# Kernel optimization log

Hardware: AMD Instinct MI355X
Metric: run time of the kernel (lower is better)

## Reference

```python
import jax, jax.numpy as jnp
import numpy as np


def setup_inputs() -> dict:
    N, E, D = 50000, 800000, 64
    key = jax.random.key(0)
    ks = jax.random.split(key, 8)
    s = 1.0 / np.sqrt(2 * D)
    inp = {
        "node_emb": jax.random.normal(ks[0], (N, D), dtype=jnp.float32),
        "edge_index": jax.random.randint(ks[1], (2, E), 0, N, dtype=jnp.int64),
        "W1": jax.random.normal(ks[2], (2 * D, D), dtype=jnp.float32) * s,
        "b1": jnp.zeros((D,), dtype=jnp.float32),
        "W2": jax.random.normal(ks[3], (D, D), dtype=jnp.float32) * (1.0 / np.sqrt(D)),
        "b2": jnp.zeros((D,), dtype=jnp.float32),
        "Wg": jax.random.normal(ks[4], (D, D), dtype=jnp.float32) * (1.0 / np.sqrt(D)),
        "bg": jnp.zeros((D,), dtype=jnp.float32),
    }
    return inp


def reference(node_emb, edge_index, W1, b1, W2, b2, Wg, bg):
    # Gather pairwise embeddings along edges
    src, dst = edge_index[0], edge_index[1]
    pair_emb = jnp.concatenate([node_emb[src], node_emb[dst]], axis=-1)  # [E, 2D]
    # Interaction MLP (dropout in eval mode -> identity)
    h = jax.nn.relu(pair_emb @ W1 + b1)
    interaction = h @ W2 + b2  # [E, D]
    # Sigmoid gate
    gate = jax.nn.sigmoid(interaction @ Wg + bg)
    gated = interaction * gate  # [E, D]
    # Scatter-mean back to source nodes
    N = node_emb.shape[0]
    summed = jax.ops.segment_sum(gated, src, num_segments=N)  # [N, D]
    counts = jax.ops.segment_sum(jnp.ones((src.shape[0],), dtype=gated.dtype), src, num_segments=N)
    pooled = summed / jnp.maximum(counts, 1.0)[:, None]
    return pooled
```

## Files before the change

### kernel.cpp

```cpp
#include <hip/hip_runtime.h>


typedef unsigned short ushort_t;
typedef __attribute__((ext_vector_type(8))) short     bf16x8;
typedef __attribute__((ext_vector_type(8))) unsigned short u16x8;
typedef __attribute__((ext_vector_type(4))) float     f32x4;

constexpr int D        = 64;
constexpr int TILE     = 64;
constexpr int BLOCK    = 256;
constexpr int PAIR_STR = 136;
constexpr int H_STR    = 72;
constexpr int G_STR    = 68;
constexpr int NFRAG    = 32;

static __device__ __forceinline__ ushort_t f2bf(float f) {
    union { float f; unsigned int u; } v; v.f = f;
    const unsigned int r = v.u + 0x7FFFu + ((v.u >> 16) & 1u);
    return (ushort_t)(r >> 16);
}


__global__ void prep_kernel(const float* __restrict__ W1, const float* __restrict__ W2,
                            const float* __restrict__ Wg,
                            const float* __restrict__ b2, const float* __restrict__ bg,
                            const float* __restrict__ emb, const int* __restrict__ ei,
                            ushort_t* __restrict__ wpack, float* __restrict__ bgp,
                            ushort_t* __restrict__ emb_bf, int* __restrict__ cnt,
                            int total_emb, int cvt_blocks, int E) {
    const int bid = blockIdx.x;
    if (bid < 64) {
        const int t = bid * 256 + threadIdx.x;
        const int f = t >> 9;
        const int l = (t >> 3) & 63;
        const int j = t & 7;
        const int k = ((f < 16) ? (f & 3) : ((f - 16) & 1)) * 32 + (l >> 4) * 8 + j;
        const int n = ((f < 16) ? (f >> 2) : (((f & 7)) >> 1)) * 16 + (l & 15);
        float v;
        if (f < 16)      v = W1[k * 64 + n];
        else if (f < 24) v = W2[k * 64 + n];
        else {
            float s = 0.f;
            const float* wr = W2 + k * 64;
#pragma unroll 8
            for (int m = 0; m < 64; ++m) s += wr[m] * Wg[m * 64 + n];
            v = s;
        }
        wpack[t] = f2bf(v);
    } else if (bid < 64 + cvt_blocks) {
        const int idx  = (bid - 64) * 256 + threadIdx.x;
        const int base = idx * 8;
        if (base < total_emb) {
            const float4 a = *(const float4*)(emb + base);
            const float4 b = *(const float4*)(emb + base + 4);
            u16x8 p;
            p[0]=f2bf(a.x); p[1]=f2bf(a.y); p[2]=f2bf(a.z); p[3]=f2bf(a.w);
            p[4]=f2bf(b.x); p[5]=f2bf(b.y); p[6]=f2bf(b.z); p[7]=f2bf(b.w);
            *(u16x8*)(emb_bf + base) = p;
        }
    } else if (bid == 64 + cvt_blocks) {
        const int n = threadIdx.x;
        if (n < 64) {
            float s = bg[n];
#pragma unroll 8
            for (int m = 0; m < 64; ++m) s += b2[m] * Wg[m * 64 + n];
            bgp[n] = s;
        }
    } else {
        const int e = ((bid - 65 - cvt_blocks) * 256 + threadIdx.x) * 4;
        if (e + 3 < E) {
            const int4 v = *(const int4*)(ei + e);
            atomicAdd(&cnt[v.x], 1); atomicAdd(&cnt[v.y], 1);
            atomicAdd(&cnt[v.z], 1); atomicAdd(&cnt[v.w], 1);
        } else {
            for (int k = e; k < E; ++k) atomicAdd(&cnt[ei[k]], 1);
        }
    }
}


__global__ void scan_block(const int* __restrict__ cnt, int* __restrict__ off,
                           int* __restrict__ bsum, int N) {
    __shared__ int s[256];
    const int t = threadIdx.x, i = blockIdx.x * 256 + t;
    const int x = (i < N) ? cnt[i] : 0;
    s[t] = x; __syncthreads();
    for (int d = 1; d < 256; d <<= 1) {
        const int v = (t >= d) ? s[t - d] : 0;
        __syncthreads();
        s[t] += v;
        __syncthreads();
    }
    if (i < N) off[i] = s[t] - x;
    if (t == 255) bsum[blockIdx.x] = s[255];
}

__global__ void scan_sums(int* __restrict__ bsum, int nb) {
    __shared__ int s[256];
    const int t = threadIdx.x;
    const int x = (t < nb) ? bsum[t] : 0;
    s[t] = x; __syncthreads();
    for (int d = 1; d < 256; d <<= 1) {
        const int v = (t >= d) ? s[t - d] : 0;
        __syncthreads();
        s[t] += v;
        __syncthreads();
    }
    if (t < nb) bsum[t] = s[t] - x;
}

__global__ void add_sums(int* __restrict__ off, const int* __restrict__ bsum, int N) {
    const int i = blockIdx.x * 256 + threadIdx.x;
    if (i < N) off[i] += bsum[blockIdx.x];
}

__global__ void scatter_idx(const int* __restrict__ ei, int* __restrict__ off,
                            int* __restrict__ sorted, int E) {
    const int e = (blockIdx.x * blockDim.x + threadIdx.x) * 4;
    if (e + 3 < E) {
        const int4 v = *(const int4*)(ei + e);
        sorted[atomicAdd(&off[v.x], 1)] = e;
        sorted[atomicAdd(&off[v.y], 1)] = e + 1;
        sorted[atomicAdd(&off[v.z], 1)] = e + 2;
        sorted[atomicAdd(&off[v.w], 1)] = e + 3;
    } else {
        for (int k = e; k < E; ++k) sorted[atomicAdd(&off[ei[k]], 1)] = k;
    }
}


__global__ __launch_bounds__(BLOCK, 5)
void edge_mlp_mfma(const ushort_t* __restrict__ emb_bf,
                   const int*   __restrict__ edge_index,
                   const int*   __restrict__ sorted,
                   const ushort_t* __restrict__ wpack,
                   const float* __restrict__ b1, const float* __restrict__ b2,
                   const float* __restrict__ bgp,
                   float* __restrict__ summed,
                   int E)
{
    __shared__ union {
        ushort_t pairA[TILE][PAIR_STR];
        float    gated[TILE][G_STR];
    } u;
    __shared__ ushort_t hA[TILE][H_STR];
    __shared__ int      srcIds[TILE];

    const int tid = threadIdx.x;

    {
        const int e = tid >> 2, q = tid & 3;
        const int ide = blockIdx.x * TILE + e;
        if (ide < E) {
            const int eg = sorted[ide];
            const int s  = edge_index[eg];
            const int dn = edge_index[E + eg];
            if (q == 0) srcIds[e] = s;
            const ushort_t* sr = emb_bf + (size_t)s  * D + q * 16;
            const ushort_t* dr = emb_bf + (size_t)dn * D + q * 16;
            *(u16x8*)&u.pairA[e][q * 16]          = *(const u16x8*)sr;
            *(u16x8*)&u.pairA[e][q * 16 + 8]      = *(const u16x8*)(sr + 8);
            *(u16x8*)&u.pairA[e][64 + q * 16]     = *(const u16x8*)dr;
            *(u16x8*)&u.pairA[e][64 + q * 16 + 8] = *(const u16x8*)(dr + 8);
        } else {
            if (q == 0) srcIds[e] = -1;
            const u16x8 z = {0,0,0,0,0,0,0,0};
            *(u16x8*)&u.pairA[e][q * 16]          = z;
            *(u16x8*)&u.pairA[e][q * 16 + 8]      = z;
            *(u16x8*)&u.pairA[e][64 + q * 16]     = z;
            *(u16x8*)&u.pairA[e][64 + q * 16 + 8] = z;
        }
    }

    const int w    = tid >> 6;
    const int ln   = tid & 63;
    const int quad = ln >> 4;
    const int cn   = ln & 15;
    const int mrow = 16 * w + cn;
    const int orow = 16 * w + quad * 4;

    bf16x8 a1f[4];
#pragma unroll
    for (int kc = 0; kc < 4; ++kc)
        a1f[kc] = *(const bf16x8*)&u.pairA[mrow][kc * 32 + quad * 8];

    f32x4 acc1[4];
#pragma unroll
    for (int nt = 0; nt < 4; ++nt) {
        const float b = b1[nt * 16 + cn];
        acc1[nt] = (f32x4){b, b, b, b};
    }
#pragma unroll
    for (int nt = 0; nt < 4; ++nt)
#pragma unroll
        for (int kc = 0; kc < 4; ++kc) {
            const bf16x8 bf = *(const bf16x8*)(wpack + ((nt * 4 + kc) * 64 + ln) * 8);
            acc1[nt] = __builtin_amdgcn_mfma_f32_16x16x32_bf16(a1f[kc], bf, acc1[nt], 0, 0, 0);
        }
#pragma unroll
    for (int nt = 0; nt < 4; ++nt)
#pragma unroll
        for (int r = 0; r < 4; ++r)
            hA[orow + r][nt * 16 + cn] = f2bf(fmaxf(acc1[nt][r], 0.f));

    bf16x8 a2f[2];
#pragma unroll
    for (int kc = 0; kc < 2; ++kc)
        a2f[kc] = *(const bf16x8*)&hA[mrow][kc * 32 + quad * 8];

    f32x4 acc2[4], accg[4];
#pragma unroll
    for (int nt = 0; nt < 4; ++nt) {
        const float b  = b2 [nt * 16 + cn];
        const float bG = bgp[nt * 16 + cn];
        acc2[nt] = (f32x4){b, b, b, b};
        accg[nt] = (f32x4){bG, bG, bG, bG};
    }
#pragma unroll
    for (int nt = 0; nt < 4; ++nt)
#pragma unroll
        for (int kc = 0; kc < 2; ++kc) {
            const bf16x8 bf2 = *(const bf16x8*)(wpack + ((16 + nt * 2 + kc) * 64 + ln) * 8);
            const bf16x8 bfg = *(const bf16x8*)(wpack + ((24 + nt * 2 + kc) * 64 + ln) * 8);
            acc2[nt] = __builtin_amdgcn_mfma_f32_16x16x32_bf16(a2f[kc], bf2, acc2[nt], 0, 0, 0);
            accg[nt] = __builtin_amdgcn_mfma_f32_16x16x32_bf16(a2f[kc], bfg, accg[nt], 0, 0, 0);
        }

#pragma unroll
    for (int nt = 0; nt < 4; ++nt)
#pragma unroll
        for (int r = 0; r < 4; ++r) {
            const float g = 1.0f / (1.0f + __expf(-accg[nt][r]));
            u.gated[orow + r][nt * 16 + cn] = acc2[nt][r] * g;
        }

    {
        const int rbase = 16 * w;
        float run = 0.f;
        int   prev = srcIds[rbase];
#pragma unroll
        for (int i = 0; i < 16; ++i) {
            const int s = srcIds[rbase + i];
            const float v = u.gated[rbase + i][ln];
            if (s != prev) {
                if (prev >= 0) unsafeAtomicAdd(&summed[(size_t)prev * D + ln], run);
                run = 0.f;
                prev = s;
            }
            run += v;
        }
        if (prev >= 0) unsafeAtomicAdd(&summed[(size_t)prev * D + ln], run);
    }
}

__global__ void finalize_mean(float* __restrict__ out,
                              const int* __restrict__ cnt,
                              int total)
{
    const int b = (blockIdx.x * blockDim.x + threadIdx.x) * 4;
    if (b < total) {
        float4 v = *(float4*)&out[b];
        const float c = fmaxf((float)cnt[b >> 6], 1.0f);
        v.x /= c; v.y /= c; v.z /= c; v.w /= c;
        *(float4*)&out[b] = v;
    }
}

extern "C" void kernel_launch(void* const* d_in, const int* in_sizes, int n_in,
                              void* d_out, int out_size, void* d_ws, size_t ws_size,
                              hipStream_t stream) {
    const float* node_emb   = (const float*)d_in[0];
    const int*   edge_index = (const int*)d_in[1];
    const float* W1 = (const float*)d_in[2];
    const float* b1 = (const float*)d_in[3];
    const float* W2 = (const float*)d_in[4];
    const float* b2 = (const float*)d_in[5];
    const float* Wg = (const float*)d_in[6];
    const float* bg = (const float*)d_in[7];

    const int N = in_sizes[0] / D;
    const int E = in_sizes[1] / 2;
    const int total_emb = N * D;

    int* cnt    = (int*)d_ws;
    int* off    = cnt + N;
    int* bsum   = off + N;
    int* sorted = bsum + 256;
    float* bgp  = (float*)(sorted + E);
    ushort_t* wpack  = (ushort_t*)(bgp + 64);
    ushort_t* emb_bf = wpack + NFRAG * 512;

    float* summed = (float*)d_out;

    hipMemsetAsync(cnt, 0, sizeof(int) * (size_t)N, stream);
    hipMemsetAsync(summed, 0, sizeof(float) * (size_t)total_emb, stream);

    const int cvt_blocks = (total_emb / 8 + 255) / 256;
    const int e4blocks   = ((E + 3) / 4 + 255) / 256;
    prep_kernel<<<64 + cvt_blocks + 1 + e4blocks, 256, 0, stream>>>(
        W1, W2, Wg, b2, bg, node_emb, edge_index,
        wpack, bgp, emb_bf, cnt, total_emb, cvt_blocks, E);

    const int nblocks = (N + 255) / 256;
    scan_block <<<nblocks, 256, 0, stream>>>(cnt, off, bsum, N);
    scan_sums  <<<1,       256, 0, stream>>>(bsum, nblocks);
    add_sums   <<<nblocks, 256, 0, stream>>>(off, bsum, N);
    scatter_idx<<<e4blocks, 256, 0, stream>>>(edge_index, off, sorted, E);

    const int ntiles = (E + TILE - 1) / TILE;
    edge_mlp_mfma<<<ntiles, BLOCK, 0, stream>>>(emb_bf, edge_index, sorted, wpack,
                                                b1, b2, bgp, summed, E);

    finalize_mean<<<(total_emb / 4 + 255) / 256, 256, 0, stream>>>(summed, cnt, total_emb);
}
```

Measured before the change: 263.0 us.

## Fuse scan passes into scatter, fold mean into edge kernel, shrink LDS per warp

Removes the scan_sums and add_sums kernels: each scatter_idx block now recomputes the block-sum prefix in shared memory and adds it to the per-block local offset. The finalize_mean pass is dropped by scaling each partial sum by the reciprocal source count before the atomic add. The edge MLP's shared memory becomes per-warp slabs reused for pair, hidden and gated data, and launch bounds rise from 5 to 8 blocks to allow more occupancy. This trades several launches and one full pass over the output for redundant per-block scans and possible register pressure.

```diff
diff --git a/kernel.cpp b/kernel.cpp
--- a/kernel.cpp
+++ b/kernel.cpp
@@ -9,10 +9,11 @@
 constexpr int D        = 64;
 constexpr int TILE     = 64;
 constexpr int BLOCK    = 256;
+constexpr int NFRAG    = 32;
+constexpr int SLAB_B   = 4352;
 constexpr int PAIR_STR = 136;
 constexpr int H_STR    = 72;
 constexpr int G_STR    = 68;
-constexpr int NFRAG    = 32;
 
 static __device__ __forceinline__ ushort_t f2bf(float f) {
     union { float f; unsigned int u; } v; v.f = f;
@@ -95,80 +96,75 @@
     if (t == 255) bsum[blockIdx.x] = s[255];
 }
 
-__global__ void scan_sums(int* __restrict__ bsum, int nb) {
-    __shared__ int s[256];
+__global__ void scatter_idx(const int* __restrict__ ei, int* __restrict__ off,
+                            const int* __restrict__ bsum, int* __restrict__ sorted,
+                            int E, int nb) {
+    __shared__ int pref[256];
     const int t = threadIdx.x;
     const int x = (t < nb) ? bsum[t] : 0;
-    s[t] = x; __syncthreads();
+    pref[t] = x; __syncthreads();
     for (int d = 1; d < 256; d <<= 1) {
-        const int v = (t >= d) ? s[t - d] : 0;
-        __syncthreads();
-        s[t] += v;
-        __syncthreads();
-    }
-    if (t < nb) bsum[t] = s[t] - x;
-}
-
-__global__ void add_sums(int* __restrict__ off, const int* __restrict__ bsum, int N) {
-    const int i = blockIdx.x * 256 + threadIdx.x;
-    if (i < N) off[i] += bsum[blockIdx.x];
-}
-
-__global__ void scatter_idx(const int* __restrict__ ei, int* __restrict__ off,
-                            int* __restrict__ sorted, int E) {
-    const int e = (blockIdx.x * blockDim.x + threadIdx.x) * 4;
+        const int v = (t >= d) ? pref[t - d] : 0;
+        __syncthreads();
+        pref[t] += v;
+        __syncthreads();
+    }
+    const int e = (blockIdx.x * blockDim.x + t) * 4;
     if (e + 3 < E) {
         const int4 v = *(const int4*)(ei + e);
-        sorted[atomicAdd(&off[v.x], 1)] = e;
-        sorted[atomicAdd(&off[v.y], 1)] = e + 1;
-        sorted[atomicAdd(&off[v.z], 1)] = e + 2;
-        sorted[atomicAdd(&off[v.w], 1)] = e + 3;
+        const int bx = v.x >> 8, by = v.y >> 8, bz = v.z >> 8, bw = v.w >> 8;
+        sorted[(bx ? pref[bx - 1] : 0) + atomicAdd(&off[v.x], 1)] = e;
+        sorted[(by ? pref[by - 1] : 0) + atomicAdd(&off[v.y], 1)] = e + 1;
+        sorted[(bz ? pref[bz - 1] : 0) + atomicAdd(&off[v.z], 1)] = e + 2;
+        sorted[(bw ? pref[bw - 1] : 0) + atomicAdd(&off[v.w], 1)] = e + 3;
     } else {
-        for (int k = e; k < E; ++k) sorted[atomicAdd(&off[ei[k]], 1)] = k;
-    }
-}
-
-
-__global__ __launch_bounds__(BLOCK, 5)
+        for (int k = e; k < E; ++k) {
+            const int s = ei[k], b = s >> 8;
+            sorted[(b ? pref[b - 1] : 0) + atomicAdd(&off[s], 1)] = k;
+        }
+    }
+}
+
+
+__global__ __launch_bounds__(BLOCK, 8)
 void edge_mlp_mfma(const ushort_t* __restrict__ emb_bf,
                    const int*   __restrict__ edge_index,
                    const int*   __restrict__ sorted,
                    const ushort_t* __restrict__ wpack,
                    const float* __restrict__ b1, const float* __restrict__ b2,
                    const float* __restrict__ bgp,
+                   const int*   __restrict__ cnt,
                    float* __restrict__ summed,
                    int E)
 {
-    __shared__ union {
-        ushort_t pairA[TILE][PAIR_STR];
-        float    gated[TILE][G_STR];
-    } u;
-    __shared__ ushort_t hA[TILE][H_STR];
-    __shared__ int      srcIds[TILE];
+    __shared__ char  slab[4][SLAB_B];
+    __shared__ int   srcIds[TILE];
+    __shared__ float rcS[TILE];
 
     const int tid = threadIdx.x;
 
     {
         const int e = tid >> 2, q = tid & 3;
+        ushort_t* prow = (ushort_t*)&slab[e >> 4][(e & 15) * (PAIR_STR * 2)];
         const int ide = blockIdx.x * TILE + e;
         if (ide < E) {
             const int eg = sorted[ide];
             const int s  = edge_index[eg];
             const int dn = edge_index[E + eg];
-            if (q == 0) srcIds[e] = s;
+            if (q == 0) { srcIds[e] = s; rcS[e] = 1.0f / fmaxf((float)cnt[s], 1.0f); }
             const ushort_t* sr = emb_bf + (size_t)s  * D + q * 16;
             const ushort_t* dr = emb_bf + (size_t)dn * D + q * 16;
-            *(u16x8*)&u.pairA[e][q * 16]          = *(const u16x8*)sr;
-            *(u16x8*)&u.pairA[e][q * 16 + 8]      = *(const u16x8*)(sr + 8);
-            *(u16x8*)&u.pairA[e][64 + q * 16]     = *(const u16x8*)dr;
-            *(u16x8*)&u.pairA[e][64 + q * 16 + 8] = *(const u16x8*)(dr + 8);
+            *(u16x8*)&prow[q * 16]          = *(const u16x8*)sr;
+            *(u16x8*)&prow[q * 16 + 8]      = *(const u16x8*)(sr + 8);
+            *(u16x8*)&prow[64 + q * 16]     = *(const u16x8*)dr;
+            *(u16x8*)&prow[64 + q * 16 + 8] = *(const u16x8*)(dr + 8);
         } else {
-            if (q == 0) srcIds[e] = -1;
+            if (q == 0) { srcIds[e] = -1; rcS[e] = 1.0f; }
             const u16x8 z = {0,0,0,0,0,0,0,0};
-            *(u16x8*)&u.pairA[e][q * 16]          = z;
-            *(u16x8*)&u.pairA[e][q * 16 + 8]      = z;
-            *(u16x8*)&u.pairA[e][64 + q * 16]     = z;
-            *(u16x8*)&u.pairA[e][64 + q * 16 + 8] = z;
+            *(u16x8*)&prow[q * 16]          = z;
+            *(u16x8*)&prow[q * 16 + 8]      = z;
+            *(u16x8*)&prow[64 + q * 16]     = z;
+            *(u16x8*)&prow[64 + q * 16 + 8] = z;
         }
     }
 
@@ -176,13 +172,14 @@
     const int ln   = tid & 63;
     const int quad = ln >> 4;
     const int cn   = ln & 15;
-    const int mrow = 16 * w + cn;
-    const int orow = 16 * w + quad * 4;
+    ushort_t* pairW = (ushort_t*)slab[w];
+    ushort_t* hW    = (ushort_t*)slab[w];
+    float*    gW    = (float*)   slab[w];
 
     bf16x8 a1f[4];
 #pragma unroll
     for (int kc = 0; kc < 4; ++kc)
-        a1f[kc] = *(const bf16x8*)&u.pairA[mrow][kc * 32 + quad * 8];
+        a1f[kc] = *(const bf16x8*)&pairW[cn * PAIR_STR + kc * 32 + quad * 8];
 
     f32x4 acc1[4];
 #pragma unroll
@@ -201,12 +198,12 @@
     for (int nt = 0; nt < 4; ++nt)
 #pragma unroll
         for (int r = 0; r < 4; ++r)
-            hA[orow + r][nt * 16 + cn] = f2bf(fmaxf(acc1[nt][r], 0.f));
+            hW[(quad * 4 + r) * H_STR + nt * 16 + cn] = f2bf(fmaxf(acc1[nt][r], 0.f));
 
     bf16x8 a2f[2];
 #pragma unroll
     for (int kc = 0; kc < 2; ++kc)
-        a2f[kc] = *(const bf16x8*)&hA[mrow][kc * 32 + quad * 8];
+        a2f[kc] = *(const bf16x8*)&hW[cn * H_STR + kc * 32 + quad * 8];
 
     f32x4 acc2[4], accg[4];
 #pragma unroll
@@ -231,38 +228,29 @@
 #pragma unroll
         for (int r = 0; r < 4; ++r) {
             const float g = 1.0f / (1.0f + __expf(-accg[nt][r]));
-            u.gated[orow + r][nt * 16 + cn] = acc2[nt][r] * g;
+            gW[(quad * 4 + r) * G_STR + nt * 16 + cn] = acc2[nt][r] * g;
         }
 
     {
         const int rbase = 16 * w;
         float run = 0.f;
         int   prev = srcIds[rbase];
+        int   lastIdx = rbase;
 #pragma unroll
         for (int i = 0; i < 16; ++i) {
             const int s = srcIds[rbase + i];
-            const float v = u.gated[rbase + i][ln];
+            const float v = gW[i * G_STR + ln];
             if (s != prev) {
-                if (prev >= 0) unsafeAtomicAdd(&summed[(size_t)prev * D + ln], run);
+                if (prev >= 0)
+                    unsafeAtomicAdd(&summed[(size_t)prev * D + ln], run * rcS[lastIdx]);
                 run = 0.f;
                 prev = s;
             }
             run += v;
-        }
-        if (prev >= 0) unsafeAtomicAdd(&summed[(size_t)prev * D + ln], run);
-    }
-}
-
-__global__ void finalize_mean(float* __restrict__ out,
-                              const int* __restrict__ cnt,
-                              int total)
-{
-    const int b = (blockIdx.x * blockDim.x + threadIdx.x) * 4;
-    if (b < total) {
-        float4 v = *(float4*)&out[b];
-        const float c = fmaxf((float)cnt[b >> 6], 1.0f);
-        v.x /= c; v.y /= c; v.z /= c; v.w /= c;
-        *(float4*)&out[b] = v;
+            lastIdx = rbase + i;
+        }
+        if (prev >= 0)
+            unsafeAtomicAdd(&summed[(size_t)prev * D + ln], run * rcS[lastIdx]);
     }
 }
 
@@ -303,13 +291,9 @@
 
     const int nblocks = (N + 255) / 256;
     scan_block <<<nblocks, 256, 0, stream>>>(cnt, off, bsum, N);
-    scan_sums  <<<1,       256, 0, stream>>>(bsum, nblocks);
-    add_sums   <<<nblocks, 256, 0, stream>>>(off, bsum, N);
-    scatter_idx<<<e4blocks, 256, 0, stream>>>(edge_index, off, sorted, E);
+    scatter_idx<<<e4blocks, 256, 0, stream>>>(edge_index, off, bsum, sorted, E, nblocks);
 
     const int ntiles = (E + TILE - 1) / TILE;
     edge_mlp_mfma<<<ntiles, BLOCK, 0, stream>>>(emb_bf, edge_index, sorted, wpack,
-                                                b1, b2, bgp, summed, E);
-
-    finalize_mean<<<(total_emb / 4 + 255) / 256, 256, 0, stream>>>(summed, cnt, total_emb);
-}
+                                                b1, b2, bgp, cnt, summed, E);
+}
```

Result: faster. 256.3 us (-2.5%).
